# Performance work log

Measured on AMD Instinct MI355X. Metric: run time of the kernel, lower is better.

## Reference

```python
import jax, jax.numpy as jnp
import numpy as np

K_SHARP = 10.0  # sigmoid sharpness from init kwarg k


def setup_inputs() -> dict:
    key = jax.random.key(0)
    k1, _ = jax.random.split(key)
    points = jax.random.normal(k1, (8192, 32), dtype=jnp.float32)
    # log-spaced thresholds, matching init_kwargs r_values
    r_values = jnp.asarray(np.logspace(0.0, np.log10(15.85), 16), dtype=jnp.float32)
    return {"points": points, "r_values": r_values}


def reference(points, r_values):
    n = points.shape[0]
    # pairwise euclidean distances (cdist p=2) via gram trick
    sq = jnp.sum(points * points, axis=-1)                       # [N]
    d2 = sq[:, None] + sq[None, :] - 2.0 * (points @ points.T)   # [N,N]
    d2 = jnp.maximum(d2, 0.0)
    iu = jnp.triu(jnp.ones((n, n), dtype=bool), k=1)             # strict upper triangle
    # safe sqrt: masked-out entries replaced by 1.0 (value irrelevant, avoids 0-grad issues)
    d = jnp.sqrt(jnp.where(iu, d2, 1.0))                         # [N,N]
    mask = iu & (d > 0.0)  # matches distances[distances > 0] after triu(1)
    cnt = jnp.sum(mask).astype(points.dtype)
    # one fused masked sigmoid-sum per threshold (sequential: one N*N temp at a time)
    sums = []
    for r in r_values:  # static length-16 loop over thresholds
        s = jnp.sum(jnp.where(mask, jax.nn.sigmoid(K_SHARP * (r - d)), 0.0))
        sums.append(s / cnt)
    correlation_sums = jnp.stack(sums)                           # [R]
    log_r = jnp.log(r_values)
    log_c = jnp.log(correlation_sums)
    A = jnp.stack([log_r, jnp.ones_like(log_r)], axis=1)         # [R,2]
    # full-rank least squares via normal equations (equivalent to lstsq here)
    sol = jnp.linalg.solve(A.T @ A, A.T @ log_c)                 # [slope, intercept]
    return -sol[0]
```

## Files before the change

kernel.cpp:

```cpp
#include <hip/hip_runtime.h>
#include <math.h>

#define NPTS 8192
#define DIM 32
#define TILE 128
#define NT (NPTS / TILE)
#define NTP (NT * (NT + 1) / 2)
#define NBINS 4096
#define BIN_SCALE 20.0f
#define NR 16
#define NBLK 1024
#define LROW 40

using bf16x8 = __attribute__((ext_vector_type(8))) short;
using f32x4  = __attribute__((ext_vector_type(4))) float;

__device__ __forceinline__ unsigned short f2bf(float f) {
    unsigned u = __float_as_uint(f);
    return (unsigned short)((u + 0x7fffu + ((u >> 16) & 1u)) >> 16);
}

__global__ void k_prep(const float* __restrict__ pts, unsigned* __restrict__ bp,
                       float* __restrict__ sq20, unsigned* __restrict__ cnt) {
    const int t = blockIdx.x * 256 + threadIdx.x;
    if (t < NBINS) cnt[t] = 0u;
    const int p = t >> 1, h = t & 1;
    const float4* src = (const float4*)(pts + (size_t)p * DIM + h * 16);
    const float4 v0 = src[0], v1 = src[1], v2 = src[2], v3 = src[3];
    float s = v0.x * v0.x + v0.y * v0.y + v0.z * v0.z + v0.w * v0.w
            + v1.x * v1.x + v1.y * v1.y + v1.z * v1.z + v1.w * v1.w
            + v2.x * v2.x + v2.y * v2.y + v2.z * v2.z + v2.w * v2.w
            + v3.x * v3.x + v3.y * v3.y + v3.z * v3.z + v3.w * v3.w;
    s += __shfl_xor(s, 1);
    if (!h) sq20[p] = s * BIN_SCALE;
    unsigned* dst = bp + (size_t)p * 16 + h * 8;
    dst[0] = (unsigned)f2bf(v0.x) | ((unsigned)f2bf(v0.y) << 16);
    dst[1] = (unsigned)f2bf(v0.z) | ((unsigned)f2bf(v0.w) << 16);
    dst[2] = (unsigned)f2bf(v1.x) | ((unsigned)f2bf(v1.y) << 16);
    dst[3] = (unsigned)f2bf(v1.z) | ((unsigned)f2bf(v1.w) << 16);
    dst[4] = (unsigned)f2bf(v2.x) | ((unsigned)f2bf(v2.y) << 16);
    dst[5] = (unsigned)f2bf(v2.z) | ((unsigned)f2bf(v2.w) << 16);
    dst[6] = (unsigned)f2bf(v3.x) | ((unsigned)f2bf(v3.y) << 16);
    dst[7] = (unsigned)f2bf(v3.z) | ((unsigned)f2bf(v3.w) << 16);
}


#define EPI1(ACC, SA20, GROW, DIAGQ) { \
    const float bf_ = fmaf(-40.f, ACC, (SA20) + sb20); \
    const int bin_ = (int)fminf(fmaxf(bf_, 0.f), (float)(NBINS - 1)); \
    if (!(DIAGQ) || ((GROW) < gcol)) atomicAdd(&hist[bin_], 1u); }

#define TCLOOP(DIAGQ) \
    _Pragma("unroll") \
    for (int tc = 0; tc < 8; ++tc) { \
        const bf16x8 bf = *(const bf16x8*)&Bb[(tc * 16 + l15) * LROW + lc * 8]; \
        const f32x4 z = {0.f, 0.f, 0.f, 0.f}; \
        const f32x4 d0 = __builtin_amdgcn_mfma_f32_16x16x32_bf16(a0, bf, z, 0, 0, 0); \
        const f32x4 d1 = __builtin_amdgcn_mfma_f32_16x16x32_bf16(a1, bf, z, 0, 0, 0); \
        const float sb20 = sqb[tc * 16 + l15]; \
        const int gcol = tj * TILE + tc * 16 + l15; (void)gcol; \
        EPI1(d0[0], sa00, g0 + 0, DIAGQ) EPI1(d0[1], sa01, g0 + 1, DIAGQ) \
        EPI1(d0[2], sa02, g0 + 2, DIAGQ) EPI1(d0[3], sa03, g0 + 3, DIAGQ) \
        EPI1(d1[0], sa10, g1 + 0, DIAGQ) EPI1(d1[1], sa11, g1 + 1, DIAGQ) \
        EPI1(d1[2], sa12, g1 + 2, DIAGQ) EPI1(d1[3], sa13, g1 + 3, DIAGQ) \
    }

__global__ __launch_bounds__(256)
void k_hist(const uint4* __restrict__ bp4, const float* __restrict__ sq20,
            unsigned* __restrict__ cnt) {
    __shared__ unsigned hist[NBINS];
    __shared__ unsigned short Ab[TILE * LROW];
    __shared__ unsigned short Bb[TILE * LROW];
    __shared__ float sqa[TILE], sqb[TILE];
    const int tid = threadIdx.x;
    const int lane = tid & 63, w = tid >> 6;
    const int l15 = lane & 15, lc = lane >> 4;
    for (int b = tid; b < NBINS; b += 256) hist[b] = 0u;
    const int P = gridDim.x;

    for (int tp = blockIdx.x; tp < NTP; tp += P) {
        int ti = 0, rr = tp;
        while (rr >= NT - ti) { rr -= NT - ti; ++ti; }
        const int tj = ti + rr;

        __syncthreads();
#pragma unroll
        for (int q = 0; q < 2; ++q) {
            const int g = tid + q * 256;
            const int p = g >> 2, c = g & 3;
            *(uint4*)&Ab[p * LROW + c * 8] = bp4[(size_t)ti * 512 + g];
            *(uint4*)&Bb[p * LROW + c * 8] = bp4[(size_t)tj * 512 + g];
        }
        if (tid < TILE) sqa[tid] = sq20[ti * TILE + tid];
        else if (tid < 2 * TILE) sqb[tid - TILE] = sq20[tj * TILE + (tid - TILE)];
        __syncthreads();

        const int r0 = (2 * w) * 16, r1 = r0 + 16;
        const bf16x8 a0 = *(const bf16x8*)&Ab[(r0 + l15) * LROW + lc * 8];
        const bf16x8 a1 = *(const bf16x8*)&Ab[(r1 + l15) * LROW + lc * 8];
        const float sa00 = sqa[r0 + lc * 4 + 0];
        const float sa01 = sqa[r0 + lc * 4 + 1];
        const float sa02 = sqa[r0 + lc * 4 + 2];
        const float sa03 = sqa[r0 + lc * 4 + 3];
        const float sa10 = sqa[r1 + lc * 4 + 0];
        const float sa11 = sqa[r1 + lc * 4 + 1];
        const float sa12 = sqa[r1 + lc * 4 + 2];
        const float sa13 = sqa[r1 + lc * 4 + 3];
        const int g0 = ti * TILE + r0 + lc * 4;
        const int g1 = ti * TILE + r1 + lc * 4;

        if (ti != tj) {
            TCLOOP(0)
        } else {
            TCLOOP(1)
        }
    }

    __syncthreads();
    for (int b = tid; b < NBINS; b += 256) {
        const unsigned h = hist[b];
        if (h) atomicAdd(&cnt[b], h);
    }
}

__global__ __launch_bounds__(1024)
void k_final(const unsigned* __restrict__ cnt, const float* __restrict__ rvals,
             float* __restrict__ out) {
    __shared__ double red[16][NR + 1];
    const int tid = threadIdx.x;
    float rv[NR];
#pragma unroll
    for (int t = 0; t < NR; ++t) rv[t] = rvals[t];

    double local[NR + 1];
#pragma unroll
    for (int t = 0; t <= NR; ++t) local[t] = 0.0;

#pragma unroll
    for (int q = 0; q < NBINS / 1024; ++q) {
        const int b = tid + q * 1024;
        const unsigned c = cnt[b];
        if (c) {
            const double cd = (double)c;
            local[NR] += cd;
            const float d = sqrtf(((float)b + 0.5f) / BIN_SCALE);
#pragma unroll
            for (int t = 0; t < NR; ++t) {
                const float x = 10.0f * (rv[t] - d);
                float s;
                if (x >= 0.f) s = 1.f / (1.f + __expf(-x));
                else          { const float e = __expf(x); s = e / (1.f + e); }
                local[t] += cd * (double)s;
            }
        }
    }

#pragma unroll
    for (int off = 32; off > 0; off >>= 1) {
#pragma unroll
        for (int t = 0; t <= NR; ++t)
            local[t] += __shfl_down(local[t], off);
    }
    const int wv = tid >> 6;
    if ((tid & 63) == 0) {
#pragma unroll
        for (int t = 0; t <= NR; ++t) red[wv][t] = local[t];
    }
    __syncthreads();

    if (tid == 0) {
        double sums[NR + 1];
#pragma unroll
        for (int t = 0; t <= NR; ++t) {
            double s = 0.0;
#pragma unroll
            for (int w2 = 0; w2 < 16; ++w2) s += red[w2][t];
            sums[t] = s;
        }
        const float logC = logf((float)sums[NR]);
        double Sx = 0, Sy = 0, Sxx = 0, Sxy = 0;
#pragma unroll
        for (int t = 0; t < NR; ++t) {
            const double x = (double)logf(rv[t]);
            const double y = (double)(logf((float)sums[t]) - logC);
            Sx += x; Sy += y; Sxx += x * x; Sxy += x * y;
        }
        const double R = (double)NR;
        const double slope = (R * Sxy - Sx * Sy) / (R * Sxx - Sx * Sx);
        out[0] = (float)(-slope);
    }
}

extern "C" void kernel_launch(void* const* d_in, const int* in_sizes, int n_in,
                              void* d_out, int out_size, void* d_ws, size_t ws_size,
                              hipStream_t stream) {
    const float* pts = (const float*)d_in[0];
    const float* rv  = (const float*)d_in[1];
    float* out = (float*)d_out;
    char* ws = (char*)d_ws;

    unsigned* bp = (unsigned*)ws;
    float* sq20 = (float*)(ws + 524288);
    unsigned* cnt = (unsigned*)(ws + 524288 + 32768);

    k_prep<<<64, 256, 0, stream>>>(pts, bp, sq20, cnt);
    k_hist<<<NBLK, 256, 0, stream>>>((const uint4*)bp, sq20, cnt);
    k_final<<<1, 1024, 0, stream>>>(cnt, rv, out);
}
```

Measured before the change: 57.57 us.

## Privatize LDS histogram into 8 sub-bins and prefetch next B tile

Each LDS histogram bin is split into 8 lane-indexed sub-copies so that lanes hitting the same distance bin no longer contend on one atomic address. Blocks become 512 threads with one 16-row A fragment per wave, read straight from global memory. The grid drops to 256 persistent blocks that prefetch the next B tile into registers while the current tile is processed. The 128KB histogram cuts occupancy to one block per CU and adds a reduction over sub-bins at the end.

```diff
diff --git a/kernel.cpp b/kernel.cpp
--- a/kernel.cpp
+++ b/kernel.cpp
@@ -9,7 +9,8 @@
 #define NBINS 4096
 #define BIN_SCALE 20.0f
 #define NR 16
-#define NBLK 1024
+#define NBLK 256
+#define NSUB 8
 #define LROW 40
 
 using bf16x8 = __attribute__((ext_vector_type(8))) short;
@@ -18,6 +19,12 @@
 __device__ __forceinline__ unsigned short f2bf(float f) {
     unsigned u = __float_as_uint(f);
     return (unsigned short)((u + 0x7fffu + ((u >> 16) & 1u)) >> 16);
+}
+
+__device__ __forceinline__ void tp_decode(int tp, int& ti, int& tj) {
+    int t = 0, r = tp;
+    while (r >= NT - t) { r -= NT - t; ++t; }
+    ti = t; tj = t + r;
 }
 
 __global__ void k_prep(const float* __restrict__ pts, unsigned* __restrict__ bp,
@@ -48,7 +55,7 @@
 #define EPI1(ACC, SA20, GROW, DIAGQ) { \
     const float bf_ = fmaf(-40.f, ACC, (SA20) + sb20); \
     const int bin_ = (int)fminf(fmaxf(bf_, 0.f), (float)(NBINS - 1)); \
-    if (!(DIAGQ) || ((GROW) < gcol)) atomicAdd(&hist[bin_], 1u); }
+    if (!(DIAGQ) || ((GROW) < gcol)) atomicAdd(&hist[(bin_ << 3) + sub], 1u); }
 
 #define TCLOOP(DIAGQ) \
     _Pragma("unroll") \
@@ -56,60 +63,55 @@
         const bf16x8 bf = *(const bf16x8*)&Bb[(tc * 16 + l15) * LROW + lc * 8]; \
         const f32x4 z = {0.f, 0.f, 0.f, 0.f}; \
         const f32x4 d0 = __builtin_amdgcn_mfma_f32_16x16x32_bf16(a0, bf, z, 0, 0, 0); \
-        const f32x4 d1 = __builtin_amdgcn_mfma_f32_16x16x32_bf16(a1, bf, z, 0, 0, 0); \
-        const float sb20 = sqb[tc * 16 + l15]; \
-        const int gcol = tj * TILE + tc * 16 + l15; (void)gcol; \
-        EPI1(d0[0], sa00, g0 + 0, DIAGQ) EPI1(d0[1], sa01, g0 + 1, DIAGQ) \
-        EPI1(d0[2], sa02, g0 + 2, DIAGQ) EPI1(d0[3], sa03, g0 + 3, DIAGQ) \
-        EPI1(d1[0], sa10, g1 + 0, DIAGQ) EPI1(d1[1], sa11, g1 + 1, DIAGQ) \
-        EPI1(d1[2], sa12, g1 + 2, DIAGQ) EPI1(d1[3], sa13, g1 + 3, DIAGQ) \
-    }
-
-__global__ __launch_bounds__(256)
+        const float sb20 = sq20[ctj * TILE + tc * 16 + l15]; \
+        const int gcol = ctj * TILE + tc * 16 + l15; (void)gcol; \
+        EPI1(d0[0], sa0, g0 + 0, DIAGQ) EPI1(d0[1], sa1, g0 + 1, DIAGQ) \
+        EPI1(d0[2], sa2, g0 + 2, DIAGQ) EPI1(d0[3], sa3, g0 + 3, DIAGQ) \
+    }
+
+__global__ __launch_bounds__(512)
 void k_hist(const uint4* __restrict__ bp4, const float* __restrict__ sq20,
             unsigned* __restrict__ cnt) {
-    __shared__ unsigned hist[NBINS];
-    __shared__ unsigned short Ab[TILE * LROW];
+    __shared__ unsigned hist[NBINS * NSUB];
     __shared__ unsigned short Bb[TILE * LROW];
-    __shared__ float sqa[TILE], sqb[TILE];
     const int tid = threadIdx.x;
     const int lane = tid & 63, w = tid >> 6;
     const int l15 = lane & 15, lc = lane >> 4;
-    for (int b = tid; b < NBINS; b += 256) hist[b] = 0u;
+    const int sub = lane & 7;
+    {
+        uint4* h4 = (uint4*)hist;
+        const uint4 z4 = {0u, 0u, 0u, 0u};
+        for (int i = tid; i < NBINS * NSUB / 4; i += 512) h4[i] = z4;
+    }
     const int P = gridDim.x;
-
-    for (int tp = blockIdx.x; tp < NTP; tp += P) {
-        int ti = 0, rr = tp;
-        while (rr >= NT - ti) { rr -= NT - ti; ++ti; }
-        const int tj = ti + rr;
-
+    const bf16x8* bpv = (const bf16x8*)bp4;
+
+    int tp = blockIdx.x;
+    int ti, tj;
+    tp_decode(tp, ti, tj);
+    uint4 reg = bp4[(size_t)tj * 512 + tid];
+
+    while (tp < NTP) {
         __syncthreads();
-#pragma unroll
-        for (int q = 0; q < 2; ++q) {
-            const int g = tid + q * 256;
-            const int p = g >> 2, c = g & 3;
-            *(uint4*)&Ab[p * LROW + c * 8] = bp4[(size_t)ti * 512 + g];
-            *(uint4*)&Bb[p * LROW + c * 8] = bp4[(size_t)tj * 512 + g];
-        }
-        if (tid < TILE) sqa[tid] = sq20[ti * TILE + tid];
-        else if (tid < 2 * TILE) sqb[tid - TILE] = sq20[tj * TILE + (tid - TILE)];
+        {   const int p = tid >> 2, c = tid & 3;
+            *(uint4*)&Bb[p * LROW + c * 8] = reg; }
         __syncthreads();
-
-        const int r0 = (2 * w) * 16, r1 = r0 + 16;
-        const bf16x8 a0 = *(const bf16x8*)&Ab[(r0 + l15) * LROW + lc * 8];
-        const bf16x8 a1 = *(const bf16x8*)&Ab[(r1 + l15) * LROW + lc * 8];
-        const float sa00 = sqa[r0 + lc * 4 + 0];
-        const float sa01 = sqa[r0 + lc * 4 + 1];
-        const float sa02 = sqa[r0 + lc * 4 + 2];
-        const float sa03 = sqa[r0 + lc * 4 + 3];
-        const float sa10 = sqa[r1 + lc * 4 + 0];
-        const float sa11 = sqa[r1 + lc * 4 + 1];
-        const float sa12 = sqa[r1 + lc * 4 + 2];
-        const float sa13 = sqa[r1 + lc * 4 + 3];
-        const int g0 = ti * TILE + r0 + lc * 4;
-        const int g1 = ti * TILE + r1 + lc * 4;
-
-        if (ti != tj) {
+        const int cti = ti, ctj = tj;
+        tp += P;
+        if (tp < NTP) {
+            tp_decode(tp, ti, tj);
+            reg = bp4[(size_t)tj * 512 + tid];
+        }
+
+        const int base_a = cti * TILE + w * 16;
+        const bf16x8 a0 = bpv[(size_t)(base_a + l15) * 4 + lc];
+        const float sa0 = sq20[base_a + lc * 4 + 0];
+        const float sa1 = sq20[base_a + lc * 4 + 1];
+        const float sa2 = sq20[base_a + lc * 4 + 2];
+        const float sa3 = sq20[base_a + lc * 4 + 3];
+        const int g0 = base_a + lc * 4;
+
+        if (cti != ctj) {
             TCLOOP(0)
         } else {
             TCLOOP(1)
@@ -117,8 +119,10 @@
     }
 
     __syncthreads();
-    for (int b = tid; b < NBINS; b += 256) {
-        const unsigned h = hist[b];
+    for (int b = tid; b < NBINS; b += 512) {
+        const uint4 h0 = *(const uint4*)&hist[b * 8];
+        const uint4 h1 = *(const uint4*)&hist[b * 8 + 4];
+        const unsigned h = h0.x + h0.y + h0.z + h0.w + h1.x + h1.y + h1.z + h1.w;
         if (h) atomicAdd(&cnt[b], h);
     }
 }
@@ -204,6 +208,6 @@
     unsigned* cnt = (unsigned*)(ws + 524288 + 32768);
 
     k_prep<<<64, 256, 0, stream>>>(pts, bp, sq20, cnt);
-    k_hist<<<NBLK, 256, 0, stream>>>((const uint4*)bp, sq20, cnt);
+    k_hist<<<NBLK, 512, 0, stream>>>((const uint4*)bp, sq20, cnt);
     k_final<<<1, 1024, 0, stream>>>(cnt, rv, out);
 }
```

Measured after the change: 52.20 us, median of 2. 9.3% less time.
